# Kernel tuning notes

Measured on AMD Instinct MI355X. Metric: run time of the kernel, lower is better.

Reference implementation:

```python
import jax, jax.numpy as jnp
import numpy as np

NUM_HEADS = 8
HEAD_CH = 8  # channels // num_heads = 64 // 8
WINDOW = 2
JOINTS = 25  # joints+bones adjacency dim


def _sym_norm_adj(a):
    d = a.sum(axis=1)
    dinv = np.where(d > 0, 1.0 / np.sqrt(d), 0.0)
    return (a * dinv[:, None]) * dinv[None, :]


def _build_global_attn():
    rng = np.random.RandomState(0)
    a = (rng.rand(JOINTS, JOINTS) < 0.15).astype(np.float32)
    a = np.maximum(a, a.T)
    np.fill_diagonal(a, 1.0)  # joints_bones_adjacency(True): self loops
    wadj = np.tile(a, (WINDOW, WINDOW))  # [V, V], V = WINDOW*JOINTS
    wadj = _sym_norm_adj(wadj)
    return jnp.asarray(wadj, jnp.float32)[None, None]  # [1,1,V,V]


def setup_inputs() -> dict:
    key = jax.random.key(0)
    ks = jax.random.split(key, 12)
    N, C, T, V = 32, 64, 256, WINDOW * JOINTS
    s = 0.05
    return {
        "x_q": jax.random.normal(ks[0], (N, C, T, V), jnp.float32),
        "x_kv": jax.random.normal(ks[1], (N, C, T, V), jnp.float32),
        "q_w": jax.random.normal(ks[2], (C, C), jnp.float32) * s,
        "q_b": jax.random.normal(ks[3], (C,), jnp.float32) * s,
        "k_w": jax.random.normal(ks[4], (C, C), jnp.float32) * s,
        "k_b": jax.random.normal(ks[5], (C,), jnp.float32) * s,
        "v_w": jax.random.normal(ks[6], (C, C), jnp.float32) * s,
        "v_b": jax.random.normal(ks[7], (C,), jnp.float32) * s,
        "o_w": jax.random.normal(ks[8], (C, C * NUM_HEADS), jnp.float32) * s,
        "o_b": jax.random.normal(ks[9], (C,), jnp.float32) * s,
        "alphas": jnp.ones((1, NUM_HEADS, 1, 1), jnp.float32),
        "global_attn": _build_global_attn(),
    }


def _conv1x1(x, w, b):
    # nn.Conv2d(kernel_size=1): y[n,o,t,v] = sum_c w[o,c] * x[n,c,t,v] + b[o]
    return jnp.einsum('nctv,oc->notv', x, w) + b[None, :, None, None]


def reference(x_q, x_kv, q_w, q_b, k_w, k_b, v_w, v_b, o_w, o_b, alphas, global_attn):
    N, C, T, V = x_q.shape
    H, hc = NUM_HEADS, HEAD_CH
    q = _conv1x1(x_q, q_w, q_b).reshape(N, H, hc, T, V)
    k = _conv1x1(x_kv, k_w, k_b).reshape(N, H, hc, T, V)
    v = _conv1x1(x_kv, v_w, v_b)  # [N, C, T, V] (full channels, not per-head)
    # tanh-scaled attention + graph bias (eval mode: dropout/head-drop inactive)
    scores = jnp.einsum('nsctu,nsctv->nsuv', q, k) / (hc * T)
    attn = jnp.tanh(scores) * alphas + global_attn  # [N, H, V, V]
    values = jnp.einsum('nctu,nsuv->nsctv', v, attn)  # [N, H, C, T, V]
    values = values.reshape(N, H * C, T, V)
    out = _conv1x1(values, o_w, o_b)  # o_proj: in = C*H, out = C
    return out
```

## Files before the change

kernel.cpp:

```cpp
#include <hip/hip_runtime.h>


__global__ void k0_prep(const float* __restrict__ qw, const float* __restrict__ kw,
                        const float* __restrict__ vw, const float* __restrict__ vb,
                        const float* __restrict__ ow,
                        float* __restrict__ wT, float* __restrict__ W2T,
                        float* __restrict__ ovb)
{
    int i = threadIdx.x + blockIdx.x * 256;
    if (i < 4096){
        int o = i >> 6, c = i & 63;
        wT[c*64 + o]        = qw[i];
        wT[4096 + c*64 + o] = kw[i];
    } else if (i < 36864){
        int j = i - 4096;
        int s = j >> 12, o = (j >> 6) & 63, a = j & 63;
        float acc = 0.f;
        for (int c = 0; c < 64; ++c)
            acc += ow[o*512 + s*64 + c] * vw[c*64 + a];
        W2T[s*4096 + a*64 + o] = acc;
    } else if (i < 37376){
        int j = i - 36864;
        int s = j >> 6, o = j & 63;
        float acc = 0.f;
        for (int c = 0; c < 64; ++c)
            acc += ow[o*512 + s*64 + c] * vb[c];
        ovb[j] = acc;
    }
}

__global__ __launch_bounds__(256, 2) void k1_qk(
    const float* __restrict__ xq, const float* __restrict__ xkv,
    const float* __restrict__ wT,
    const float* __restrict__ qb, const float* __restrict__ kb,
    float* __restrict__ qo, float* __restrict__ ko, int n0)
{
    __shared__ float sx[64*256];
    const int nrel = blockIdx.y;
    const int nabs = n0 + nrel;
    const int p0   = blockIdx.x * 256;
    const int tid  = threadIdx.x;
    const size_t abase = (size_t)nabs * 819200;
    const size_t rbase = (size_t)nrel * 819200;

    for (int phase = 0; phase < 2; ++phase){
        const float* src  = phase ? xkv : xq;
        const float* bias = phase ? kb : qb;
        const float* w    = phase ? (wT + 4096) : wT;

        if (phase) __syncthreads();
        {
            const float* g = src + abase + p0;
            #pragma unroll
            for (int j = 0; j < 16; ++j){
                int i4 = tid + j*256;
                int c = i4 >> 6, m4 = i4 & 63;
                float4 val = *(const float4*)(g + (size_t)c*12800 + m4*4);
                *(float4*)(&sx[c*256 + m4*4]) = val;
            }
        }
        __syncthreads();

        for (int h = 0; h < 2; ++h){
            const int o0 = h*32;
            float acc[32];
            #pragma unroll
            for (int j = 0; j < 32; ++j) acc[j] = bias[o0+j];
            for (int c = 0; c < 64; ++c){
                float xv = sx[c*256 + tid];
                const float* row = w + c*64 + o0;
                #pragma unroll
                for (int j = 0; j < 32; ++j) acc[j] += row[j] * xv;
            }
            float* dst = phase ? (ko + abase) : (qo + rbase);
            #pragma unroll
            for (int j = 0; j < 32; ++j)
                dst[(size_t)(o0+j)*12800 + p0 + tid] = acc[j];
        }
    }
}

__global__ __launch_bounds__(256, 2) void k2_partial(
    const float* __restrict__ qc, const float* __restrict__ kd,
    float* __restrict__ pscore, int n0)
{
    __shared__ float red[4*2500];
    const int bid  = blockIdx.x;
    const int kq   = bid & 3;
    const int s    = (bid >> 2) & 7;
    const int nrel = bid >> 5;
    const int tid  = threadIdx.x;
    const int wave = __builtin_amdgcn_readfirstlane(tid >> 6);
    const int lane = tid & 63;
    const float* qf = qc + (size_t)nrel * 819200 + (size_t)s * 102400;
    const float* kf = kd + (size_t)(n0 + nrel) * 819200 + (size_t)s * 102400;

    float acc[50];
    #pragma unroll
    for (int w = 0; w < 50; ++w) acc[w] = 0.f;

    if (lane < 50){
        const int r0 = kq*512 + wave*128;
        for (int kk = r0; kk < r0 + 128; kk += 4){
            float qv[4];
            #pragma unroll
            for (int t = 0; t < 4; ++t) qv[t] = qf[(size_t)(kk+t)*50 + lane];
            #pragma unroll
            for (int t = 0; t < 4; ++t){
                const float* kr = kf + (size_t)(kk+t)*50;
                #pragma unroll
                for (int w = 0; w < 50; ++w) acc[w] += qv[t] * kr[w];
            }
        }
        #pragma unroll
        for (int w = 0; w < 50; ++w) red[wave*2500 + lane*50 + w] = acc[w];
    }
    __syncthreads();

    for (int i = tid; i < 2500; i += 256)
        pscore[(size_t)bid*2500 + i] = red[i] + red[2500+i] + red[5000+i] + red[7500+i];
}

__global__ void k2_final(const float* __restrict__ pscore,
                         const float* __restrict__ alphas, const float* __restrict__ gattn,
                         float* __restrict__ attnc)
{
    const int b = blockIdx.x;
    const int s = b & 7;
    const float inv = 1.0f / 2048.0f;
    const float alpha = alphas[s];
    for (int i = threadIdx.x; i < 2500; i += 256){
        float sum = pscore[(size_t)(b*4+0)*2500 + i] + pscore[(size_t)(b*4+1)*2500 + i]
                  + pscore[(size_t)(b*4+2)*2500 + i] + pscore[(size_t)(b*4+3)*2500 + i];
        attnc[(size_t)b*2500 + i] = tanhf(sum * inv) * alpha + gattn[i];
    }
}

__global__ __launch_bounds__(256, 1) void k3_out(
    const float* __restrict__ xkv, const float* __restrict__ attnc,
    const float* __restrict__ W2T, const float* __restrict__ ovb,
    const float* __restrict__ ob, float* __restrict__ out, int n0)
{
    extern __shared__ float lds[];
    float* sx   = lds;
    float* sp   = lds + 16384;
    float* sw2t = lds + 29184;
    float* sa   = lds + 33280;
    float* sovb = lds + 36480;

    const int nrel = blockIdx.y;
    const int tb   = blockIdx.x;
    const int tid  = threadIdx.x;
    const int tloc = __builtin_amdgcn_readfirstlane(tid >> 6);
    const int lane = tid & 63;
    const int WL   = lane >> 3;
    const int WS   = lane & 7;
    const int trow = tb*4 + tloc;
    const size_t abase = (size_t)(n0 + nrel) * 819200;

    {
        const float4* xg = (const float4*)(xkv + abase + (size_t)tb*200);
        for (int i4 = tid; i4 < 3200; i4 += 256){
            int a = i4 / 50, r = i4 - a*50;
            float4 v = xg[(size_t)a*3200 + r];
            int g0 = r*4;
            #pragma unroll
            for (int e = 0; e < 4; ++e){
                int g = g0 + e;
                int tt = g / 50, u = g - tt*50;
                sx[(tt*64 + a)*64 + u] = ((const float*)&v)[e];
            }
        }
        {
            int tt = tid >> 6, a = tid & 63;
            float* row = sx + (tt*64 + a)*64;
            #pragma unroll
            for (int c = 50; c < 64; ++c) row[c] = 0.f;
        }
        sovb[tid]       = ovb[tid];
        sovb[tid + 256] = ovb[tid + 256];
    }

    float acc2[8][8];
    #pragma unroll
    for (int ro = 0; ro < 8; ++ro)
        #pragma unroll
        for (int rw = 0; rw < 8; ++rw) acc2[ro][rw] = 0.f;

    const float* xw = sx + tloc*4096 + 8*WS;
    const float* wt = sw2t + 8*WL;
    char*        pb8 = (char*)(sp + tloc*3200);
    const float* aw = sa + 8*WS;

    for (int s = 0; s < 8; ++s){
        __syncthreads();
        {
            const float4* g4 = (const float4*)(W2T + s*4096);
            float4* d4 = (float4*)sw2t;
            #pragma unroll
            for (int it = 0; it < 4; ++it) d4[tid + it*256] = g4[tid + it*256];

            const float* ag = attnc + (size_t)(nrel*8 + s)*2500;
            for (int i = tid; i < 3200; i += 256){
                int u = i >> 6, w = i & 63;
                sa[i] = (w < 50) ? ag[u*50 + w] : 0.f;
            }
        }
        __syncthreads();

        float acc1[8][8];
        {
            float pbv[8];
            #pragma unroll
            for (int ro = 0; ro < 8; ++ro) pbv[ro] = sovb[s*64 + 8*WL + ro];
            #pragma unroll
            for (int ro = 0; ro < 8; ++ro)
                #pragma unroll
                for (int rm = 0; rm < 8; ++rm) acc1[ro][rm] = pbv[ro];
        }
        #pragma unroll 2
        for (int a = 0; a < 64; ++a){
            float wv[8], xv[8];
            *(float4*)&wv[0] = *(const float4*)(wt + a*64);
            *(float4*)&wv[4] = *(const float4*)(wt + a*64 + 4);
            *(float4*)&xv[0] = *(const float4*)(xw + a*64);
            *(float4*)&xv[4] = *(const float4*)(xw + a*64 + 4);
            #pragma unroll
            for (int ro = 0; ro < 8; ++ro)
                #pragma unroll
                for (int rm = 0; rm < 8; ++rm)
                    acc1[ro][rm] = fmaf(wv[ro], xv[rm], acc1[ro][rm]);
        }

        #pragma unroll
        for (int rm = 0; rm < 8; ++rm){
            const int u = 8*WS + rm;
            if (u < 50){
                char* row = pb8 + u*256;
                const int xo = 16*WS;
                *(float4*)(row + ((32*WL +  0) ^ xo)) =
                    make_float4(acc1[0][rm], acc1[1][rm], acc1[2][rm], acc1[3][rm]);
                *(float4*)(row + ((32*WL + 16) ^ xo)) =
                    make_float4(acc1[4][rm], acc1[5][rm], acc1[6][rm], acc1[7][rm]);
            }
        }

        #pragma unroll 2
        for (int u = 0; u < 50; ++u){
            const int xo = 16*(u >> 3);
            float pv[8], av[8];
            *(float4*)&pv[0] = *(const float4*)(pb8 + u*256 + ((32*WL +  0) ^ xo));
            *(float4*)&pv[4] = *(const float4*)(pb8 + u*256 + ((32*WL + 16) ^ xo));
            *(float4*)&av[0] = *(const float4*)(aw + u*64);
            *(float4*)&av[4] = *(const float4*)(aw + u*64 + 4);
            #pragma unroll
            for (int ro = 0; ro < 8; ++ro)
                #pragma unroll
                for (int rw = 0; rw < 8; ++rw)
                    acc2[ro][rw] = fmaf(pv[ro], av[rw], acc2[ro][rw]);
        }
    }

    #pragma unroll
    for (int ro = 0; ro < 8; ++ro){
        const int o = 8*WL + ro;
        const float b = ob[o];
        float* op = out + abase + (size_t)o*12800 + trow*50;
        #pragma unroll
        for (int j = 0; j < 4; ++j){
            const int w0 = 8*WS + 2*j;
            if (w0 <= 48)
                *(float2*)(op + w0) = make_float2(acc2[ro][2*j]   + b,
                                                  acc2[ro][2*j+1] + b);
        }
    }
}

extern "C" void kernel_launch(void* const* d_in, const int* in_sizes, int n_in,
                              void* d_out, int out_size, void* d_ws, size_t ws_size,
                              hipStream_t stream)
{
    const float* x_q    = (const float*)d_in[0];
    const float* x_kv   = (const float*)d_in[1];
    const float* q_w    = (const float*)d_in[2];
    const float* q_b    = (const float*)d_in[3];
    const float* k_w    = (const float*)d_in[4];
    const float* k_b    = (const float*)d_in[5];
    const float* v_w    = (const float*)d_in[6];
    const float* v_b    = (const float*)d_in[7];
    const float* o_w    = (const float*)d_in[8];
    const float* o_b    = (const float*)d_in[9];
    const float* alphas = (const float*)d_in[10];
    const float* gattn  = (const float*)d_in[11];
    float* out = (float*)d_out;

    char* ws = (char*)d_ws;
    float* qchunk = (float*)(ws);
    float* pscore = (float*)(ws + 26214400);
    float* attnc  = (float*)(ws + 28774400);
    float* wT     = (float*)(ws + 29414400);
    float* W2T    = (float*)(ws + 29447168);
    float* ovb    = (float*)(ws + 29578240);

    hipFuncSetAttribute((const void*)k3_out,
                        hipFuncAttributeMaxDynamicSharedMemorySize, 147968);

    k0_prep<<<146, 256, 0, stream>>>(q_w, k_w, v_w, v_b, o_w, wT, W2T, ovb);

    for (int g = 0; g < 4; ++g){
        const int n0 = g * 8;
        k1_qk<<<dim3(50, 8), 256, 0, stream>>>(x_q, x_kv, wT, q_b, k_b,
                                               qchunk, out , n0);
        k2_partial<<<256, 256, 0, stream>>>(qchunk, (const float*)d_out, pscore, n0);
        k2_final<<<64, 256, 0, stream>>>(pscore, alphas, gattn, attnc);
        k3_out<<<dim3(64, 8), 256, 147968, stream>>>(x_kv, attnc, W2T, ovb, o_b, out, n0);
    }
}
```

Measured before the change: 1.688 ms.

## Split k3_out heads across wave pairs with global operand reads and LDS reduction

k3_out now processes 2 time rows per block instead of 4. The four waves split the 8 heads into two halves, and an LDS reduction combines the two halves of the accumulator before the output is written. W2T, attn and the output bias are read directly from global/cache instead of being staged in LDS for each head. This removes the per-head __syncthreads barriers and cuts LDS use from about 148KB to 78KB, so two blocks can be resident per CU, and the grid doubles. The cost is higher global/L2 load traffic in the inner loops and an extra reduction step. The attn matrix is also padded to 52-wide rows so it can be loaded with float4.

```diff
diff --git a/kernel.cpp b/kernel.cpp
--- a/kernel.cpp
+++ b/kernel.cpp
@@ -132,54 +132,47 @@
     for (int i = threadIdx.x; i < 2500; i += 256){
         float sum = pscore[(size_t)(b*4+0)*2500 + i] + pscore[(size_t)(b*4+1)*2500 + i]
                   + pscore[(size_t)(b*4+2)*2500 + i] + pscore[(size_t)(b*4+3)*2500 + i];
-        attnc[(size_t)b*2500 + i] = tanhf(sum * inv) * alpha + gattn[i];
-    }
-}
-
-__global__ __launch_bounds__(256, 1) void k3_out(
+        int u = i / 50, w = i - u*50;
+        attnc[(size_t)b*2600 + u*52 + w] = tanhf(sum * inv) * alpha + gattn[i];
+    }
+}
+
+__global__ __launch_bounds__(256, 2) void k3_out(
     const float* __restrict__ xkv, const float* __restrict__ attnc,
     const float* __restrict__ W2T, const float* __restrict__ ovb,
     const float* __restrict__ ob, float* __restrict__ out, int n0)
 {
     extern __shared__ float lds[];
-    float* sx   = lds;
-    float* sp   = lds + 16384;
-    float* sw2t = lds + 29184;
-    float* sa   = lds + 33280;
-    float* sovb = lds + 36480;
+    float* sx = lds;
+    float* sp = lds + 6656;
 
     const int nrel = blockIdx.y;
     const int tb   = blockIdx.x;
     const int tid  = threadIdx.x;
-    const int tloc = __builtin_amdgcn_readfirstlane(tid >> 6);
+    const int wv   = __builtin_amdgcn_readfirstlane(tid >> 6);
     const int lane = tid & 63;
+    const int tloc = wv & 1;
+    const int sh   = wv >> 1;
     const int WL   = lane >> 3;
     const int WS   = lane & 7;
-    const int trow = tb*4 + tloc;
+    const int trow = tb*2 + tloc;
     const size_t abase = (size_t)(n0 + nrel) * 819200;
 
     {
-        const float4* xg = (const float4*)(xkv + abase + (size_t)tb*200);
-        for (int i4 = tid; i4 < 3200; i4 += 256){
-            int a = i4 / 50, r = i4 - a*50;
-            float4 v = xg[(size_t)a*3200 + r];
-            int g0 = r*4;
+        const float4* xg = (const float4*)(xkv + abase);
+        for (int i4 = tid; i4 < 1600; i4 += 256){
+            int a = i4 / 25, j = i4 - a*25;
+            float4 v = xg[(size_t)a*3200 + tb*25 + j];
+            int g0 = j*4;
             #pragma unroll
             for (int e = 0; e < 4; ++e){
                 int g = g0 + e;
-                int tt = g / 50, u = g - tt*50;
-                sx[(tt*64 + a)*64 + u] = ((const float*)&v)[e];
-            }
-        }
-        {
-            int tt = tid >> 6, a = tid & 63;
-            float* row = sx + (tt*64 + a)*64;
-            #pragma unroll
-            for (int c = 50; c < 64; ++c) row[c] = 0.f;
-        }
-        sovb[tid]       = ovb[tid];
-        sovb[tid + 256] = ovb[tid + 256];
-    }
+                int tt = (g >= 50) ? 1 : 0;
+                sx[tt*3328 + a*52 + (g - tt*50)] = ((const float*)&v)[e];
+            }
+        }
+    }
+    __syncthreads();
 
     float acc2[8][8];
     #pragma unroll
@@ -187,49 +180,36 @@
         #pragma unroll
         for (int rw = 0; rw < 8; ++rw) acc2[ro][rw] = 0.f;
 
-    const float* xw = sx + tloc*4096 + 8*WS;
-    const float* wt = sw2t + 8*WL;
-    char*        pb8 = (char*)(sp + tloc*3200);
-    const float* aw = sa + 8*WS;
-
-    for (int s = 0; s < 8; ++s){
-        __syncthreads();
-        {
-            const float4* g4 = (const float4*)(W2T + s*4096);
-            float4* d4 = (float4*)sw2t;
-            #pragma unroll
-            for (int it = 0; it < 4; ++it) d4[tid + it*256] = g4[tid + it*256];
-
-            const float* ag = attnc + (size_t)(nrel*8 + s)*2500;
-            for (int i = tid; i < 3200; i += 256){
-                int u = i >> 6, w = i & 63;
-                sa[i] = (w < 50) ? ag[u*50 + w] : 0.f;
-            }
-        }
-        __syncthreads();
+    const float* xw  = sx + tloc*3328 + 8*WS;
+    char*        pb8 = (char*)(sp + wv*3200);
+    const float* agb = attnc + (size_t)(nrel*8)*2600 + 8*WS;
+
+    for (int si = 0; si < 4; ++si){
+        const int s = sh*4 + si;
 
         float acc1[8][8];
         {
             float pbv[8];
-            #pragma unroll
-            for (int ro = 0; ro < 8; ++ro) pbv[ro] = sovb[s*64 + 8*WL + ro];
+            *(float4*)&pbv[0] = *(const float4*)(ovb + s*64 + 8*WL);
+            *(float4*)&pbv[4] = *(const float4*)(ovb + s*64 + 8*WL + 4);
             #pragma unroll
             for (int ro = 0; ro < 8; ++ro)
                 #pragma unroll
                 for (int rm = 0; rm < 8; ++rm) acc1[ro][rm] = pbv[ro];
         }
+        const float* wS = W2T + s*4096 + 8*WL;
         #pragma unroll 2
         for (int a = 0; a < 64; ++a){
-            float wv[8], xv[8];
-            *(float4*)&wv[0] = *(const float4*)(wt + a*64);
-            *(float4*)&wv[4] = *(const float4*)(wt + a*64 + 4);
-            *(float4*)&xv[0] = *(const float4*)(xw + a*64);
-            *(float4*)&xv[4] = *(const float4*)(xw + a*64 + 4);
+            float wvx[8], xv[8];
+            *(float4*)&wvx[0] = *(const float4*)(wS + a*64);
+            *(float4*)&wvx[4] = *(const float4*)(wS + a*64 + 4);
+            *(float4*)&xv[0]  = *(const float4*)(xw + a*52);
+            *(float4*)&xv[4]  = *(const float4*)(xw + a*52 + 4);
             #pragma unroll
             for (int ro = 0; ro < 8; ++ro)
                 #pragma unroll
                 for (int rm = 0; rm < 8; ++rm)
-                    acc1[ro][rm] = fmaf(wv[ro], xv[rm], acc1[ro][rm]);
+                    acc1[ro][rm] = fmaf(wvx[ro], xv[rm], acc1[ro][rm]);
         }
 
         #pragma unroll
@@ -245,14 +225,15 @@
             }
         }
 
+        const float* aS = agb + (size_t)s*2600;
         #pragma unroll 2
         for (int u = 0; u < 50; ++u){
             const int xo = 16*(u >> 3);
             float pv[8], av[8];
             *(float4*)&pv[0] = *(const float4*)(pb8 + u*256 + ((32*WL +  0) ^ xo));
             *(float4*)&pv[4] = *(const float4*)(pb8 + u*256 + ((32*WL + 16) ^ xo));
-            *(float4*)&av[0] = *(const float4*)(aw + u*64);
-            *(float4*)&av[4] = *(const float4*)(aw + u*64 + 4);
+            *(float4*)&av[0] = *(const float4*)(aS + u*52);
+            *(float4*)&av[4] = *(const float4*)(aS + u*52 + 4);
             #pragma unroll
             for (int ro = 0; ro < 8; ++ro)
                 #pragma unroll
@@ -261,17 +242,39 @@
         }
     }
 
-    #pragma unroll
-    for (int ro = 0; ro < 8; ++ro){
-        const int o = 8*WL + ro;
-        const float b = ob[o];
-        float* op = out + abase + (size_t)o*12800 + trow*50;
-        #pragma unroll
-        for (int j = 0; j < 4; ++j){
-            const int w0 = 8*WS + 2*j;
-            if (w0 <= 48)
-                *(float2*)(op + w0) = make_float2(acc2[ro][2*j]   + b,
-                                                  acc2[ro][2*j+1] + b);
+    __syncthreads();
+    float* red = lds;
+    if (sh == 1){
+        float* r = red + (tloc*64 + lane)*68;
+        #pragma unroll
+        for (int j = 0; j < 16; ++j){
+            const int ro = (4*j) >> 3, rw = (4*j) & 7;
+            *(float4*)(r + 4*j) = make_float4(acc2[ro][rw],   acc2[ro][rw+1],
+                                              acc2[ro][rw+2], acc2[ro][rw+3]);
+        }
+    }
+    __syncthreads();
+    if (sh == 0){
+        const float* r = red + (tloc*64 + lane)*68;
+        #pragma unroll
+        for (int j = 0; j < 16; ++j){
+            const int ro = (4*j) >> 3, rw = (4*j) & 7;
+            float4 rv = *(const float4*)(r + 4*j);
+            acc2[ro][rw]   += rv.x;  acc2[ro][rw+1] += rv.y;
+            acc2[ro][rw+2] += rv.z;  acc2[ro][rw+3] += rv.w;
+        }
+        #pragma unroll
+        for (int ro = 0; ro < 8; ++ro){
+            const int o = 8*WL + ro;
+            const float b = ob[o];
+            float* op = out + abase + (size_t)o*12800 + trow*50;
+            #pragma unroll
+            for (int j = 0; j < 4; ++j){
+                const int w0 = 8*WS + 2*j;
+                if (w0 <= 48)
+                    *(float2*)(op + w0) = make_float2(acc2[ro][2*j]   + b,
+                                                      acc2[ro][2*j+1] + b);
+            }
         }
     }
 }
@@ -298,12 +301,12 @@
     float* qchunk = (float*)(ws);
     float* pscore = (float*)(ws + 26214400);
     float* attnc  = (float*)(ws + 28774400);
-    float* wT     = (float*)(ws + 29414400);
-    float* W2T    = (float*)(ws + 29447168);
-    float* ovb    = (float*)(ws + 29578240);
+    float* wT     = (float*)(ws + 29440000);
+    float* W2T    = (float*)(ws + 29472768);
+    float* ovb    = (float*)(ws + 29603840);
 
     hipFuncSetAttribute((const void*)k3_out,
-                        hipFuncAttributeMaxDynamicSharedMemorySize, 147968);
+                        hipFuncAttributeMaxDynamicSharedMemorySize, 77824);
 
     k0_prep<<<146, 256, 0, stream>>>(q_w, k_w, v_w, v_b, o_w, wT, W2T, ovb);
 
@@ -313,6 +316,6 @@
                                                qchunk, out , n0);
         k2_partial<<<256, 256, 0, stream>>>(qchunk, (const float*)d_out, pscore, n0);
         k2_final<<<64, 256, 0, stream>>>(pscore, alphas, gattn, attnc);
-        k3_out<<<dim3(64, 8), 256, 147968, stream>>>(x_kv, attnc, W2T, ovb, o_b, out, n0);
-    }
-}
+        k3_out<<<dim3(128, 8), 256, 77824, stream>>>(x_kv, attnc, W2T, ovb, o_b, out, n0);
+    }
+}
```

New measurement: 1.429 ms. 1.18x faster.
